# Kernel optimization log

Measured on AMD Instinct MI355X. Metric: run time of the kernel, lower is better.

Reference implementation:

```python
import jax, jax.numpy as jnp
import numpy as np

B, S, D, H = 4, 2048, 1024, 16
HD = D // H  # head_dim = 64


def setup_inputs() -> dict:
    key = jax.random.key(0)
    ks = jax.random.split(key, 9)
    sc = 0.02
    return {
        "x": jax.random.normal(ks[0], (B, S, D), dtype=jnp.float32),
        "mask": jnp.zeros((B, S), dtype=bool),  # True = masked
        "Wq": jax.random.normal(ks[1], (D, D), dtype=jnp.float32) * sc,
        "bq": jnp.zeros((D,), dtype=jnp.float32),
        "Wk": jax.random.normal(ks[2], (D, D), dtype=jnp.float32) * sc,
        "bk": jnp.zeros((D,), dtype=jnp.float32),
        "Wv": jax.random.normal(ks[3], (D, D), dtype=jnp.float32) * sc,
        "bv": jnp.zeros((D,), dtype=jnp.float32),
        "Wo": jax.random.normal(ks[4], (D, D), dtype=jnp.float32) * sc,
        "bo": jnp.zeros((D,), dtype=jnp.float32),
    }


def reference(x, mask, Wq, bq, Wk, bk, Wv, bv, Wo, bo):
    b, s, _ = x.shape
    scale = HD ** -0.5
    # projections, split heads: (b, h, s, hd)
    def heads(t):
        return t.reshape(b, s, H, HD).transpose(0, 2, 1, 3)
    q = heads(x @ Wq + bq)
    k = heads(x @ Wk + bk)
    v = heads(x @ Wv + bv)
    # scores: (b, h, s, s)
    attn = jnp.einsum('bhqd,bhkd->bhqk', q, k) * scale
    attn = jnp.where(mask[:, None, None, :], -jnp.inf, attn)
    attn = jax.nn.softmax(attn, axis=-1)
    # dropout p=0.0 -> identity (eval parity)
    out = jnp.einsum('bhqk,bhkd->bhqd', attn, v)
    out = out.transpose(0, 2, 1, 3).reshape(b, s, D)
    return out @ Wo + bo
```

## Files before the change

kernel.cpp:

```cpp
#include <hip/hip_runtime.h>
#include <cstdint>


typedef __bf16 bf16x8 __attribute__((ext_vector_type(8)));
typedef __bf16 bf16x4v __attribute__((ext_vector_type(4)));
typedef float f32x4 __attribute__((ext_vector_type(4)));
typedef unsigned u32x2 __attribute__((ext_vector_type(2)));
typedef unsigned u32x4 __attribute__((ext_vector_type(4)));

#define DEV __device__ __forceinline__

#if __has_builtin(__builtin_amdgcn_exp2f)
#define EXP2(x) __builtin_amdgcn_exp2f(x)
#else
#define EXP2(x) exp2f(x)
#endif

DEV __bf16 f2bf(float f) { return (__bf16)f; }

DEV void gload16(const void* g, void* l) {
  __builtin_amdgcn_global_load_lds(
      (const __attribute__((address_space(1))) unsigned int*)(uintptr_t)g,
      (__attribute__((address_space(3))) unsigned int*)(uintptr_t)l,
      16, 0, 0);
}

__global__ __launch_bounds__(256) void f2bf_vec4(const float4* __restrict__ in,
                                                 bf16x4v* __restrict__ out, int n4) {
  int i = blockIdx.x * blockDim.x + threadIdx.x;
  int stride = gridDim.x * blockDim.x;
  for (; i < n4; i += stride) {
    float4 v = in[i];
    bf16x4v o = { f2bf(v.x), f2bf(v.y), f2bf(v.z), f2bf(v.w) };
    out[i] = o;
  }
}

__global__ __launch_bounds__(256) void pack_mask(const unsigned char* __restrict__ mask,
                                                 unsigned* __restrict__ pm) {
  int t = threadIdx.x;
  int b = t >> 6, tile = (t >> 1) & 31, half = t & 1;
  unsigned bits = 0;
  for (int j = 0; j < 32; ++j)
    if (mask[b * 2048 + tile * 64 + half * 32 + j]) bits |= (1u << j);
  pm[b * 64 + tile * 2 + half] = bits;
}

__global__ __launch_bounds__(256) void pack_bias(const float* __restrict__ bq,
                                                 const float* __restrict__ bk,
                                                 const float* __restrict__ bv,
                                                 float* __restrict__ pb, float qs) {
  int i = blockIdx.x * 256 + threadIdx.x;
  float v = (i < 1024) ? bq[i] * qs : (i < 2048) ? bk[i - 1024] : bv[i - 2048];
  pb[i] = v;
}

__global__ __launch_bounds__(256) void transpose_w4(const float* __restrict__ w0,
                                                    const float* __restrict__ w1,
                                                    const float* __restrict__ w2,
                                                    const float* __restrict__ w3,
                                                    __bf16* __restrict__ dstb, float qs) {
  __shared__ float tile[32][33];
  const int which = blockIdx.z;
  const float* src = which == 0 ? w0 : which == 1 ? w1 : which == 2 ? w2 : w3;
  const float scale = (which == 0) ? qs : 1.0f;
  __bf16* dst = dstb + (size_t)which * 1024 * 1024;
  const int tx = threadIdx.x & 31;
  const int ty = threadIdx.x >> 5;
  const int x0 = blockIdx.x * 32;
  const int y0 = blockIdx.y * 32;
#pragma unroll
  for (int j = 0; j < 4; ++j)
    tile[ty + j * 8][tx] = src[(size_t)(y0 + ty + j * 8) * 1024 + x0 + tx];
  __syncthreads();
#pragma unroll
  for (int j = 0; j < 4; ++j)
    dst[(size_t)(x0 + ty + j * 8) * 1024 + y0 + tx] = f2bf(tile[tx][ty + j * 8] * scale);
}

__global__ __launch_bounds__(256, 2) void gemm128(const __bf16* __restrict__ A,
                                                  const __bf16* __restrict__ Bt,
                                                  const float* __restrict__ bias,
                                                  void* __restrict__ o0, void* __restrict__ o1,
                                                  void* __restrict__ o2, int mode) {
  constexpr int K = 1024;
  __shared__ alignas(16) __bf16 S[32768];
  const int t = threadIdx.x;
  const int lane = t & 63, w = t >> 6;
  const int g = lane >> 4, c = lane & 15;
  const int sw = c & 7;
  const int wm = w & 1, wn = w >> 1;
  const int bid = blockIdx.x;
  const int j = bid >> 3;
  const int m0 = (((bid & 7) << 3) + (j & 7)) << 7;
  const int n0 = (j >> 3) << 7;

  float bb4[4];
#pragma unroll
  for (int jj = 0; jj < 4; ++jj) bb4[jj] = bias[n0 + wn * 64 + jj * 16 + c];
  asm volatile("" :: "v"(bb4[0]), "v"(bb4[1]), "v"(bb4[2]), "v"(bb4[3]) : "memory");

  f32x4 acc[4][4];
#pragma unroll
  for (int i = 0; i < 4; ++i)
#pragma unroll
    for (int jj = 0; jj < 4; ++jj) acc[i][jj] = f32x4{0.f, 0.f, 0.f, 0.f};

  auto stage = [&](int bb, int k0) {
#pragma unroll
    for (int r2 = 0; r2 < 4; ++r2) {
      int slot = r2 * 256 + t;
      int row = slot >> 3, ch = slot & 7;
      int gch = ch ^ (row & 7);
      gload16(&A[(size_t)(m0 + row) * K + k0 + gch * 8], &S[bb * 8192 + slot * 8]);
      gload16(&Bt[(size_t)(n0 + row) * K + k0 + gch * 8], &S[16384 + bb * 8192 + slot * 8]);
    }
  };

  asm volatile("s_waitcnt vmcnt(0)" ::: "memory");
  stage(0, 0);

#pragma unroll 1
  for (int kt = 0; kt < 16; ++kt) {
    const int bb = kt & 1;
    if (kt < 15) {
      stage(bb ^ 1, (kt + 1) << 6);
      asm volatile("s_waitcnt vmcnt(8)" ::: "memory");
    } else {
      asm volatile("s_waitcnt vmcnt(0)" ::: "memory");
    }
    __builtin_amdgcn_s_barrier();

    const __bf16* As_ = S + bb * 8192;
    const __bf16* Bs_ = S + 16384 + bb * 8192;
    __builtin_amdgcn_s_setprio(1);
#pragma unroll
    for (int kk = 0; kk < 2; ++kk) {
      bf16x8 af[4], bfr[4];
#pragma unroll
      for (int i = 0; i < 4; ++i) {
        af[i]  = *(const bf16x8*)&As_[(wm * 64 + i * 16 + c) * 64 + (((kk * 4 + g) ^ sw) << 3)];
        bfr[i] = *(const bf16x8*)&Bs_[(wn * 64 + i * 16 + c) * 64 + (((kk * 4 + g) ^ sw) << 3)];
      }
#pragma unroll
      for (int i = 0; i < 4; ++i)
#pragma unroll
        for (int jj = 0; jj < 4; ++jj)
          acc[i][jj] = __builtin_amdgcn_mfma_f32_16x16x32_bf16(af[i], bfr[jj], acc[i][jj], 0, 0, 0);
    }
    __builtin_amdgcn_s_setprio(0);
    __builtin_amdgcn_s_barrier();
  }

  const int bidx = m0 >> 11;
  const int s0g = m0 & 2047;

  if (mode == 2) {
#pragma unroll
    for (int i = 0; i < 4; ++i) {
      const int rowb = m0 + wm * 64 + i * 16 + g * 4;
#pragma unroll
      for (int jj = 0; jj < 4; ++jj) {
        const int col = n0 + wn * 64 + jj * 16 + c;
#pragma unroll
        for (int r = 0; r < 4; ++r)
          ((float*)o0)[(size_t)(rowb + r) * 1024 + col] = acc[i][jj][r] + bb4[jj];
      }
    }
    return;
  }

  const int seg = n0 >> 10;
  const int hb = (n0 & 1023) >> 6;
  unsigned short* LB = (unsigned short*)S;

#pragma unroll
  for (int hh = 0; hh < 2; ++hh) {
    __syncthreads();
    if (wn == hh) {
#pragma unroll
      for (int i = 0; i < 4; ++i) {
        const int rl = wm * 64 + i * 16 + g * 4;
#pragma unroll
        for (int jj = 0; jj < 4; ++jj) {
          const int col = jj * 16 + c;
#pragma unroll
          for (int r = 0; r < 4; ++r) {
            const int row = rl + r;
            __bf16 v = f2bf(acc[i][jj][r] + bb4[jj]);
            if (seg < 2) {
              LB[row * 72 + col] = __builtin_bit_cast(unsigned short, v);
            } else {
              int spl = (row & 0x63) | ((row & 0x10) >> 2) | ((row & 0x0C) << 1);
              LB[col * 136 + spl] = __builtin_bit_cast(unsigned short, v);
            }
          }
        }
      }
    }
    __syncthreads();
    if (seg < 2) {
      __bf16* dst = (__bf16*)(seg == 0 ? o0 : o1);
      const size_t hbase = ((size_t)(bidx * 16 + hb + hh) * 2048 + s0g) * 64;
#pragma unroll
      for (int s4 = 0; s4 < 4; ++s4) {
        int row = s4 * 32 + (t >> 3);
        int hd0 = (t & 7) * 8;
        bf16x8 v = *(const bf16x8*)&LB[row * 72 + hd0];
        *(bf16x8*)&dst[hbase + (size_t)row * 64 + hd0] = v;
      }
    } else {
      __bf16* dst = (__bf16*)o2;
      const int hd = t >> 2, q4 = t & 3;
      const size_t vb = ((size_t)(bidx * 16 + hb + hh) * 64 + hd) * 2048 + s0g;
#pragma unroll
      for (int kk = 0; kk < 4; ++kk) {
        int spb = q4 * 32 + kk * 8;
        bf16x8 v = *(const bf16x8*)&LB[hd * 136 + spb];
        *(bf16x8*)&dst[vb + spb] = v;
      }
    }
  }
}

__global__ __launch_bounds__(256, 4) void attn_kernel(const __bf16* __restrict__ q,
                                                      const __bf16* __restrict__ k,
                                                      const __bf16* __restrict__ vt,
                                                      const unsigned* __restrict__ pm,
                                                      __bf16* __restrict__ outp) {
  const int bid = blockIdx.x;
  const int xcd = bid & 7, j = bid >> 3;
  const int bh = xcd * 8 + (j & 7), qb = j >> 3;
  const int b = bh >> 4, h = bh & 15;
  const int t = threadIdx.x, lane = t & 63, w = t >> 6;
  const int g = lane >> 4, c = lane & 15;
  const int sw = c & 7;

  __shared__ alignas(16) __bf16 S[12288];
  __bf16* Vs = S + 8192;

  const size_t kbase = (size_t)bh * (2048 * 64);
  const size_t vbase = (size_t)bh * (64 * 2048);
  const int q0 = qb * 128 + w * 32;

  unsigned mword = pm[b * 64 + lane];

  bf16x8 qf[2][2];
#pragma unroll
  for (int i = 0; i < 2; ++i)
#pragma unroll
    for (int m = 0; m < 2; ++m)
      qf[i][m] = *(const bf16x8*)&q[kbase + (size_t)(q0 + i * 16 + c) * 64 + m * 32 + g * 8];
  asm volatile("" :: "v"(qf[0][0]), "v"(qf[0][1]), "v"(qf[1][0]), "v"(qf[1][1]),
                     "v"(mword) : "memory");

  f32x4 acc[2][4];
  f32x4 lacc[2];
#pragma unroll
  for (int i = 0; i < 2; ++i) {
    lacc[i] = f32x4{0.f, 0.f, 0.f, 0.f};
#pragma unroll
    for (int n = 0; n < 4; ++n) acc[i][n] = f32x4{0.f, 0.f, 0.f, 0.f};
  }

  const bf16x8 ones = { (__bf16)1.f, (__bf16)1.f, (__bf16)1.f, (__bf16)1.f,
                        (__bf16)1.f, (__bf16)1.f, (__bf16)1.f, (__bf16)1.f };

  auto stageK = [&](int bb, int kv0) {
#pragma unroll
    for (int r2 = 0; r2 < 2; ++r2) {
      int slot = r2 * 256 + t;
      int row = slot >> 3, ch = slot & 7;
      int gch = ch ^ (row & 7);
      gload16(&k[kbase + (size_t)(kv0 + row) * 64 + gch * 8], &S[bb * 4096 + slot * 8]);
    }
  };
  auto stageV = [&](int kv0) {
#pragma unroll
    for (int r2 = 0; r2 < 2; ++r2) {
      int slot = r2 * 256 + t;
      int row = slot >> 3, ch = slot & 7;
      int gch = ch ^ (row & 7);
      gload16(&vt[vbase + (size_t)row * 2048 + kv0 + gch * 8], &Vs[slot * 8]);
    }
  };

  stageK(0, 0);
  stageV(0);

#pragma unroll 1
  for (int kv = 0; kv < 32; ++kv) {
    const int bb = kv & 1;
    const int kv0 = kv << 6;
    if (kv < 31) {
      stageK(bb ^ 1, kv0 + 64);
      asm volatile("s_waitcnt vmcnt(2)" ::: "memory");
    } else {
      asm volatile("s_waitcnt vmcnt(0)" ::: "memory");
    }
    __builtin_amdgcn_s_barrier();

    const __bf16* ksb = S + (bb << 12);
    unsigned mwlo = __builtin_amdgcn_readlane(mword, 2 * kv);
    unsigned mwhi = __builtin_amdgcn_readlane(mword, 2 * kv + 1);

    __builtin_amdgcn_s_setprio(1);
    f32x4 sc[2][4];
#pragma unroll
    for (int n = 0; n < 4; ++n) {
      bf16x8 kf0 = *(const bf16x8*)&ksb[(n * 16 + c) * 64 + (((0 + g) ^ sw) << 3)];
      bf16x8 kf1 = *(const bf16x8*)&ksb[(n * 16 + c) * 64 + (((4 + g) ^ sw) << 3)];
#pragma unroll
      for (int i = 0; i < 2; ++i) {
        f32x4 z = f32x4{0.f, 0.f, 0.f, 0.f};
        z = __builtin_amdgcn_mfma_f32_16x16x32_bf16(kf0, qf[i][0], z, 0, 0, 0);
        z = __builtin_amdgcn_mfma_f32_16x16x32_bf16(kf1, qf[i][1], z, 0, 0, 0);
        sc[i][n] = z;
      }
    }
    __builtin_amdgcn_sched_barrier(0);

    u32x4 pf0[2];
    if (mwlo) {
#pragma unroll
      for (int n = 0; n < 2; ++n)
#pragma unroll
        for (int r = 0; r < 4; ++r)
          if ((mwlo >> (n * 16 + g * 4 + r)) & 1u) { sc[0][n][r] = -1e30f; sc[1][n][r] = -1e30f; }
    }
#pragma unroll
    for (int i = 0; i < 2; ++i) {
      float p0 = EXP2(sc[i][0][0]), p1 = EXP2(sc[i][0][1]);
      float p2 = EXP2(sc[i][0][2]), p3 = EXP2(sc[i][0][3]);
      float p4 = EXP2(sc[i][1][0]), p5 = EXP2(sc[i][1][1]);
      float p6 = EXP2(sc[i][1][2]), p7 = EXP2(sc[i][1][3]);
      unsigned w0, w1, w2, w3;
      asm("v_cvt_pk_bf16_f32 %0, %1, %2" : "=v"(w0) : "v"(p0), "v"(p1));
      asm("v_cvt_pk_bf16_f32 %0, %1, %2" : "=v"(w1) : "v"(p2), "v"(p3));
      asm("v_cvt_pk_bf16_f32 %0, %1, %2" : "=v"(w2) : "v"(p4), "v"(p5));
      asm("v_cvt_pk_bf16_f32 %0, %1, %2" : "=v"(w3) : "v"(p6), "v"(p7));
      pf0[i] = u32x4{w0, w1, w2, w3};
    }

#pragma unroll
    for (int n = 0; n < 4; ++n) {
      bf16x8 vf0 = *(const bf16x8*)&Vs[(n * 16 + c) * 64 + (((0 + g) ^ sw) << 3)];
#pragma unroll
      for (int i = 0; i < 2; ++i)
        acc[i][n] = __builtin_amdgcn_mfma_f32_16x16x32_bf16(vf0, __builtin_bit_cast(bf16x8, pf0[i]), acc[i][n], 0, 0, 0);
    }
#pragma unroll
    for (int i = 0; i < 2; ++i)
      lacc[i] = __builtin_amdgcn_mfma_f32_16x16x32_bf16(ones, __builtin_bit_cast(bf16x8, pf0[i]), lacc[i], 0, 0, 0);
    __builtin_amdgcn_sched_barrier(0);

    u32x4 pf1[2];
    if (mwhi) {
#pragma unroll
      for (int n = 2; n < 4; ++n)
#pragma unroll
        for (int r = 0; r < 4; ++r)
          if ((mwhi >> ((n - 2) * 16 + g * 4 + r)) & 1u) { sc[0][n][r] = -1e30f; sc[1][n][r] = -1e30f; }
    }
#pragma unroll
    for (int i = 0; i < 2; ++i) {
      float p0 = EXP2(sc[i][2][0]), p1 = EXP2(sc[i][2][1]);
      float p2 = EXP2(sc[i][2][2]), p3 = EXP2(sc[i][2][3]);
      float p4 = EXP2(sc[i][3][0]), p5 = EXP2(sc[i][3][1]);
      float p6 = EXP2(sc[i][3][2]), p7 = EXP2(sc[i][3][3]);
      unsigned w0, w1, w2, w3;
      asm("v_cvt_pk_bf16_f32 %0, %1, %2" : "=v"(w0) : "v"(p0), "v"(p1));
      asm("v_cvt_pk_bf16_f32 %0, %1, %2" : "=v"(w1) : "v"(p2), "v"(p3));
      asm("v_cvt_pk_bf16_f32 %0, %1, %2" : "=v"(w2) : "v"(p4), "v"(p5));
      asm("v_cvt_pk_bf16_f32 %0, %1, %2" : "=v"(w3) : "v"(p6), "v"(p7));
      pf1[i] = u32x4{w0, w1, w2, w3};
    }

#pragma unroll
    for (int n = 0; n < 4; ++n) {
      bf16x8 vf1 = *(const bf16x8*)&Vs[(n * 16 + c) * 64 + (((4 + g) ^ sw) << 3)];
#pragma unroll
      for (int i = 0; i < 2; ++i)
        acc[i][n] = __builtin_amdgcn_mfma_f32_16x16x32_bf16(vf1, __builtin_bit_cast(bf16x8, pf1[i]), acc[i][n], 0, 0, 0);
    }
#pragma unroll
    for (int i = 0; i < 2; ++i)
      lacc[i] = __builtin_amdgcn_mfma_f32_16x16x32_bf16(ones, __builtin_bit_cast(bf16x8, pf1[i]), lacc[i], 0, 0, 0);
    __builtin_amdgcn_s_setprio(0);

    __builtin_amdgcn_s_barrier();
    if (kv < 31) stageV(kv0 + 64);
  }

  float linv[2];
#pragma unroll
  for (int i = 0; i < 2; ++i) linv[i] = 1.0f / fmaxf(lacc[i][0], 1e-30f);

  __bf16* ot = S + w * 2176;
#pragma unroll
  for (int i = 0; i < 2; ++i)
#pragma unroll
    for (int n = 0; n < 4; ++n) {
      float a0 = acc[i][n][0] * linv[i], a1 = acc[i][n][1] * linv[i];
      float a2 = acc[i][n][2] * linv[i], a3 = acc[i][n][3] * linv[i];
      unsigned w0, w1;
      asm("v_cvt_pk_bf16_f32 %0, %1, %2" : "=v"(w0) : "v"(a0), "v"(a1));
      asm("v_cvt_pk_bf16_f32 %0, %1, %2" : "=v"(w1) : "v"(a2), "v"(a3));
      *(u32x2*)&ot[(i * 16 + c) * 68 + n * 16 + g * 4] = u32x2{w0, w1};
    }
  asm volatile("s_waitcnt lgkmcnt(0)" ::: "memory");
  __builtin_amdgcn_sched_barrier(0);
#pragma unroll
  for (int ps = 0; ps < 4; ++ps) {
    int rr = ps * 8 + (lane >> 3);
    bf16x8 ov = *(const bf16x8*)&ot[rr * 68 + (lane & 7) * 8];
    *(bf16x8*)&outp[((size_t)b * 2048 + q0 + rr) * 1024 + h * 64 + (lane & 7) * 8] = ov;
  }
}

extern "C" void kernel_launch(void* const* d_in, const int* in_sizes, int n_in,
                              void* d_out, int out_size, void* d_ws, size_t ws_size,
                              hipStream_t stream) {
  (void)in_sizes; (void)n_in; (void)out_size; (void)ws_size;
  const float* x  = (const float*)d_in[0];
  const unsigned char* mask = (const unsigned char*)d_in[1];
  const float* Wq = (const float*)d_in[2];
  const float* bq = (const float*)d_in[3];
  const float* Wk = (const float*)d_in[4];
  const float* bk = (const float*)d_in[5];
  const float* Wv = (const float*)d_in[6];
  const float* bv = (const float*)d_in[7];
  const float* Wo = (const float*)d_in[8];
  const float* bo = (const float*)d_in[9];
  float* out = (float*)d_out;

  char* ws = (char*)d_ws;
  const size_t SZ = (size_t)8192 * 1024 * 2;
  const size_t WSZ = (size_t)1024 * 1024 * 2;
  __bf16* xb  = (__bf16*)(ws);
  __bf16* qb  = (__bf16*)(ws + SZ);
  __bf16* kb  = (__bf16*)(ws + 2 * SZ);
  __bf16* vtb = (__bf16*)(ws + 3 * SZ);
  __bf16* wtq = (__bf16*)(ws + 4 * SZ);
  __bf16* wto = (__bf16*)(ws + 4 * SZ + 3 * WSZ);
  unsigned* pmask = (unsigned*)(ws + 4 * SZ + 4 * WSZ);
  float* pb = (float*)(ws + 4 * SZ + 4 * WSZ + 4096);

  const float QSCALE = 0.125f * 1.44269504f;

  f2bf_vec4<<<2048, 256, 0, stream>>>((const float4*)x, (bf16x4v*)xb, 8192 * 1024 / 4);
  pack_mask<<<1, 256, 0, stream>>>(mask, pmask);
  pack_bias<<<12, 256, 0, stream>>>(bq, bk, bv, pb, QSCALE);
  transpose_w4<<<dim3(32, 32, 4), 256, 0, stream>>>(Wq, Wk, Wv, Wo, wtq, QSCALE);
  gemm128<<<dim3(1536), 256, 0, stream>>>(xb, wtq, pb, qb, kb, vtb, 3);
  attn_kernel<<<dim3(1024), 256, 0, stream>>>(qb, kb, vtb, pmask, xb);
  gemm128<<<dim3(512), 256, 0, stream>>>(xb, wto, bo, out, nullptr, nullptr, 2);
}
```

Before: 180.3 us.

## Switch GEMMs to 256x128 tiles with 512 threads and triple-buffered LDS

Replaces the 128x128 GEMM with a 256x128 tile computed by 8 waves. It uses a three-stage LDS ring (dynamic shared memory, 144KB) and splits each K-step into four MFMA quarters, with interleaved global loads and barriers between them. The XCD-aware block mapping is rewritten around a per-GEMM column-block count, and the transposed-V epilogue is adapted to the taller tile. The aim is better operand reuse and deeper prefetch to hide load latency, at the cost of one block per CU from the LDS footprint and more barriers per K-step.

```diff
diff --git a/kernel.cpp b/kernel.cpp
--- a/kernel.cpp
+++ b/kernel.cpp
@@ -24,6 +24,8 @@
       (__attribute__((address_space(3))) unsigned int*)(uintptr_t)l,
       16, 0, 0);
 }
+
+#define MFMA16(a, b, c) __builtin_amdgcn_mfma_f32_16x16x32_bf16((a), (b), (c), 0, 0, 0)
 
 __global__ __launch_bounds__(256) void f2bf_vec4(const float4* __restrict__ in,
                                                  bf16x4v* __restrict__ out, int n4) {
@@ -78,22 +80,26 @@
     dst[(size_t)(x0 + ty + j * 8) * 1024 + y0 + tx] = f2bf(tile[tx][ty + j * 8] * scale);
 }
 
-__global__ __launch_bounds__(256, 2) void gemm128(const __bf16* __restrict__ A,
+__global__ __launch_bounds__(512, 2) void gemm256(const __bf16* __restrict__ A,
                                                   const __bf16* __restrict__ Bt,
                                                   const float* __restrict__ bias,
                                                   void* __restrict__ o0, void* __restrict__ o1,
-                                                  void* __restrict__ o2, int mode) {
+                                                  void* __restrict__ o2,
+                                                  int nbn, int mode) {
+  extern __shared__ __align__(16) char smem_raw[];
+  __bf16* S = (__bf16*)smem_raw;
   constexpr int K = 1024;
-  __shared__ alignas(16) __bf16 S[32768];
   const int t = threadIdx.x;
   const int lane = t & 63, w = t >> 6;
   const int g = lane >> 4, c = lane & 15;
   const int sw = c & 7;
-  const int wm = w & 1, wn = w >> 1;
+  const int wm = w & 3, wn = w >> 2;
   const int bid = blockIdx.x;
-  const int j = bid >> 3;
-  const int m0 = (((bid & 7) << 3) + (j & 7)) << 7;
-  const int n0 = (j >> 3) << 7;
+  const int xcd = bid & 7, j0 = bid >> 3;
+  const int mb = xcd * 4 + j0 / nbn;
+  const int nb = j0 % nbn;
+  const int m0 = mb << 8;
+  const int n0 = nb << 7;
 
   float bb4[4];
 #pragma unroll
@@ -106,54 +112,117 @@
 #pragma unroll
     for (int jj = 0; jj < 4; ++jj) acc[i][jj] = f32x4{0.f, 0.f, 0.f, 0.f};
 
-  auto stage = [&](int bb, int k0) {
-#pragma unroll
-    for (int r2 = 0; r2 < 4; ++r2) {
-      int slot = r2 * 256 + t;
-      int row = slot >> 3, ch = slot & 7;
-      int gch = ch ^ (row & 7);
-      gload16(&A[(size_t)(m0 + row) * K + k0 + gch * 8], &S[bb * 8192 + slot * 8]);
-      gload16(&Bt[(size_t)(n0 + row) * K + k0 + gch * 8], &S[16384 + bb * 8192 + slot * 8]);
+  auto stA = [&](int bufe, int k0, int h) {
+#pragma unroll
+    for (int r2 = 0; r2 < 2; ++r2) {
+      int slot = r2 * 512 + t;
+      int row = slot >> 3;
+      int gch = (slot & 7) ^ (row & 7);
+      gload16(&A[(size_t)(m0 + h * 128 + row) * K + k0 + gch * 8],
+              &S[bufe + h * 8192 + slot * 8]);
     }
   };
+  auto stB = [&](int bufe, int k0, int h) {
+    int row = t >> 3;
+    int gch = (t & 7) ^ (row & 7);
+    gload16(&Bt[(size_t)(n0 + h * 64 + row) * K + k0 + gch * 8],
+            &S[bufe + 16384 + h * 4096 + t * 8]);
+  };
 
   asm volatile("s_waitcnt vmcnt(0)" ::: "memory");
-  stage(0, 0);
+  stA(0, 0, 0); stA(0, 0, 1); stB(0, 0, 0); stB(0, 0, 1);
+  stA(24576, 64, 0); stA(24576, 64, 1); stB(24576, 64, 0); stB(24576, 64, 1);
+
+  const int arow = wm * 64 + c;
+  const int brow = wn * 64 + c;
 
 #pragma unroll 1
   for (int kt = 0; kt < 16; ++kt) {
-    const int bb = kt & 1;
-    if (kt < 15) {
-      stage(bb ^ 1, (kt + 1) << 6);
+    const int cb = (kt % 3) * 24576;
+    const int pb2 = ((kt + 2) % 3) * 24576;
+    const int k0p = (kt + 2) << 6;
+    const __bf16* Ab = S + cb;
+    const __bf16* Bb = S + cb + 16384;
+    bf16x8 af[2][2], b01[2][2], b23[2][2];
+
+    if (kt < 14) {
+      stA(pb2, k0p, 0);
       asm volatile("s_waitcnt vmcnt(8)" ::: "memory");
+    } else if (kt == 14) {
+      asm volatile("s_waitcnt vmcnt(6)" ::: "memory");
     } else {
       asm volatile("s_waitcnt vmcnt(0)" ::: "memory");
     }
     __builtin_amdgcn_s_barrier();
-
-    const __bf16* As_ = S + bb * 8192;
-    const __bf16* Bs_ = S + 16384 + bb * 8192;
+#pragma unroll
+    for (int i = 0; i < 2; ++i)
+#pragma unroll
+      for (int kk = 0; kk < 2; ++kk)
+        af[i][kk] = *(const bf16x8*)&Ab[(arow + i * 16) * 64 + (((kk * 4 + g) ^ sw) << 3)];
+#pragma unroll
+    for (int jn = 0; jn < 2; ++jn)
+#pragma unroll
+      for (int kk = 0; kk < 2; ++kk)
+        b01[jn][kk] = *(const bf16x8*)&Bb[(brow + jn * 16) * 64 + (((kk * 4 + g) ^ sw) << 3)];
     __builtin_amdgcn_s_setprio(1);
 #pragma unroll
-    for (int kk = 0; kk < 2; ++kk) {
-      bf16x8 af[4], bfr[4];
-#pragma unroll
-      for (int i = 0; i < 4; ++i) {
-        af[i]  = *(const bf16x8*)&As_[(wm * 64 + i * 16 + c) * 64 + (((kk * 4 + g) ^ sw) << 3)];
-        bfr[i] = *(const bf16x8*)&Bs_[(wn * 64 + i * 16 + c) * 64 + (((kk * 4 + g) ^ sw) << 3)];
-      }
-#pragma unroll
-      for (int i = 0; i < 4; ++i)
-#pragma unroll
-        for (int jj = 0; jj < 4; ++jj)
-          acc[i][jj] = __builtin_amdgcn_mfma_f32_16x16x32_bf16(af[i], bfr[jj], acc[i][jj], 0, 0, 0);
-    }
+    for (int kk = 0; kk < 2; ++kk)
+#pragma unroll
+      for (int i = 0; i < 2; ++i)
+#pragma unroll
+        for (int jn = 0; jn < 2; ++jn)
+          acc[i][jn] = MFMA16(af[i][kk], b01[jn][kk], acc[i][jn]);
     __builtin_amdgcn_s_setprio(0);
+
+    if (kt < 14) stA(pb2, k0p, 1);
+    asm volatile("" ::: "memory");
     __builtin_amdgcn_s_barrier();
-  }
-
-  const int bidx = m0 >> 11;
-  const int s0g = m0 & 2047;
+#pragma unroll
+    for (int jn = 0; jn < 2; ++jn)
+#pragma unroll
+      for (int kk = 0; kk < 2; ++kk)
+        b23[jn][kk] = *(const bf16x8*)&Bb[(brow + (jn + 2) * 16) * 64 + (((kk * 4 + g) ^ sw) << 3)];
+    __builtin_amdgcn_s_setprio(1);
+#pragma unroll
+    for (int kk = 0; kk < 2; ++kk)
+#pragma unroll
+      for (int i = 0; i < 2; ++i)
+#pragma unroll
+        for (int jn = 0; jn < 2; ++jn)
+          acc[i][jn + 2] = MFMA16(af[i][kk], b23[jn][kk], acc[i][jn + 2]);
+    __builtin_amdgcn_s_setprio(0);
+
+    if (kt < 14) stB(pb2, k0p, 0);
+    asm volatile("" ::: "memory");
+    __builtin_amdgcn_s_barrier();
+#pragma unroll
+    for (int i = 0; i < 2; ++i)
+#pragma unroll
+      for (int kk = 0; kk < 2; ++kk)
+        af[i][kk] = *(const bf16x8*)&Ab[(arow + (i + 2) * 16) * 64 + (((kk * 4 + g) ^ sw) << 3)];
+    __builtin_amdgcn_s_setprio(1);
+#pragma unroll
+    for (int kk = 0; kk < 2; ++kk)
+#pragma unroll
+      for (int i = 0; i < 2; ++i)
+#pragma unroll
+        for (int jn = 0; jn < 2; ++jn)
+          acc[i + 2][jn] = MFMA16(af[i][kk], b01[jn][kk], acc[i + 2][jn]);
+    __builtin_amdgcn_s_setprio(0);
+
+    if (kt < 14) stB(pb2, k0p, 1);
+    asm volatile("" ::: "memory");
+    __builtin_amdgcn_s_barrier();
+    __builtin_amdgcn_s_setprio(1);
+#pragma unroll
+    for (int kk = 0; kk < 2; ++kk)
+#pragma unroll
+      for (int i = 0; i < 2; ++i)
+#pragma unroll
+        for (int jn = 0; jn < 2; ++jn)
+          acc[i + 2][jn + 2] = MFMA16(af[i][kk], b23[jn][kk], acc[i + 2][jn + 2]);
+    __builtin_amdgcn_s_setprio(0);
+  }
 
   if (mode == 2) {
 #pragma unroll
@@ -172,6 +241,8 @@
 
   const int seg = n0 >> 10;
   const int hb = (n0 & 1023) >> 6;
+  const int bidx = m0 >> 11;
+  const int s0g = m0 & 2047;
   unsigned short* LB = (unsigned short*)S;
 
 #pragma unroll
@@ -191,8 +262,8 @@
             if (seg < 2) {
               LB[row * 72 + col] = __builtin_bit_cast(unsigned short, v);
             } else {
-              int spl = (row & 0x63) | ((row & 0x10) >> 2) | ((row & 0x0C) << 1);
-              LB[col * 136 + spl] = __builtin_bit_cast(unsigned short, v);
+              int spl = (row & ~0x1C) | ((row & 0x0C) << 1) | ((row & 0x10) >> 2);
+              LB[col * 264 + spl] = __builtin_bit_cast(unsigned short, v);
             }
           }
         }
@@ -204,20 +275,19 @@
       const size_t hbase = ((size_t)(bidx * 16 + hb + hh) * 2048 + s0g) * 64;
 #pragma unroll
       for (int s4 = 0; s4 < 4; ++s4) {
-        int row = s4 * 32 + (t >> 3);
+        int row = s4 * 64 + (t >> 3);
         int hd0 = (t & 7) * 8;
         bf16x8 v = *(const bf16x8*)&LB[row * 72 + hd0];
         *(bf16x8*)&dst[hbase + (size_t)row * 64 + hd0] = v;
       }
     } else {
       __bf16* dst = (__bf16*)o2;
-      const int hd = t >> 2, q4 = t & 3;
-      const size_t vb = ((size_t)(bidx * 16 + hb + hh) * 64 + hd) * 2048 + s0g;
-#pragma unroll
-      for (int kk = 0; kk < 4; ++kk) {
-        int spb = q4 * 32 + kk * 8;
-        bf16x8 v = *(const bf16x8*)&LB[hd * 136 + spb];
-        *(bf16x8*)&dst[vb + spb] = v;
+#pragma unroll
+      for (int p = 0; p < 4; ++p) {
+        int hd = p * 16 + (t >> 5);
+        int sl = (t & 31) * 8;
+        bf16x8 v = *(const bf16x8*)&LB[hd * 264 + sl];
+        *(bf16x8*)&dst[((size_t)(bidx * 16 + hb + hh) * 64 + hd) * 2048 + s0g + sl] = v;
       }
     }
   }
@@ -313,8 +383,8 @@
 #pragma unroll
       for (int i = 0; i < 2; ++i) {
         f32x4 z = f32x4{0.f, 0.f, 0.f, 0.f};
-        z = __builtin_amdgcn_mfma_f32_16x16x32_bf16(kf0, qf[i][0], z, 0, 0, 0);
-        z = __builtin_amdgcn_mfma_f32_16x16x32_bf16(kf1, qf[i][1], z, 0, 0, 0);
+        z = MFMA16(kf0, qf[i][0], z);
+        z = MFMA16(kf1, qf[i][1], z);
         sc[i][n] = z;
       }
     }
@@ -347,11 +417,11 @@
       bf16x8 vf0 = *(const bf16x8*)&Vs[(n * 16 + c) * 64 + (((0 + g) ^ sw) << 3)];
 #pragma unroll
       for (int i = 0; i < 2; ++i)
-        acc[i][n] = __builtin_amdgcn_mfma_f32_16x16x32_bf16(vf0, __builtin_bit_cast(bf16x8, pf0[i]), acc[i][n], 0, 0, 0);
+        acc[i][n] = MFMA16(vf0, __builtin_bit_cast(bf16x8, pf0[i]), acc[i][n]);
     }
 #pragma unroll
     for (int i = 0; i < 2; ++i)
-      lacc[i] = __builtin_amdgcn_mfma_f32_16x16x32_bf16(ones, __builtin_bit_cast(bf16x8, pf0[i]), lacc[i], 0, 0, 0);
+      lacc[i] = MFMA16(ones, __builtin_bit_cast(bf16x8, pf0[i]), lacc[i]);
     __builtin_amdgcn_sched_barrier(0);
 
     u32x4 pf1[2];
@@ -381,11 +451,11 @@
       bf16x8 vf1 = *(const bf16x8*)&Vs[(n * 16 + c) * 64 + (((4 + g) ^ sw) << 3)];
 #pragma unroll
       for (int i = 0; i < 2; ++i)
-        acc[i][n] = __builtin_amdgcn_mfma_f32_16x16x32_bf16(vf1, __builtin_bit_cast(bf16x8, pf1[i]), acc[i][n], 0, 0, 0);
+        acc[i][n] = MFMA16(vf1, __builtin_bit_cast(bf16x8, pf1[i]), acc[i][n]);
     }
 #pragma unroll
     for (int i = 0; i < 2; ++i)
-      lacc[i] = __builtin_amdgcn_mfma_f32_16x16x32_bf16(ones, __builtin_bit_cast(bf16x8, pf1[i]), lacc[i], 0, 0, 0);
+      lacc[i] = MFMA16(ones, __builtin_bit_cast(bf16x8, pf1[i]), lacc[i]);
     __builtin_amdgcn_s_setprio(0);
 
     __builtin_amdgcn_s_barrier();
@@ -447,12 +517,13 @@
   float* pb = (float*)(ws + 4 * SZ + 4 * WSZ + 4096);
 
   const float QSCALE = 0.125f * 1.44269504f;
+  const int LDSB = 147456;
 
   f2bf_vec4<<<2048, 256, 0, stream>>>((const float4*)x, (bf16x4v*)xb, 8192 * 1024 / 4);
   pack_mask<<<1, 256, 0, stream>>>(mask, pmask);
   pack_bias<<<12, 256, 0, stream>>>(bq, bk, bv, pb, QSCALE);
   transpose_w4<<<dim3(32, 32, 4), 256, 0, stream>>>(Wq, Wk, Wv, Wo, wtq, QSCALE);
-  gemm128<<<dim3(1536), 256, 0, stream>>>(xb, wtq, pb, qb, kb, vtb, 3);
+  gemm256<<<dim3(768), 512, LDSB, stream>>>(xb, wtq, pb, qb, kb, vtb, 24, 3);
   attn_kernel<<<dim3(1024), 256, 0, stream>>>(qb, kb, vtb, pmask, xb);
-  gemm128<<<dim3(512), 256, 0, stream>>>(xb, wto, bo, out, nullptr, nullptr, 2);
-}
+  gemm256<<<dim3(256), 512, LDSB, stream>>>(xb, wto, bo, out, nullptr, nullptr, 8, 2);
+}
```

Result: slower. 184.1 us (+2.1%).

## Single-buffer GEMM shared memory to raise occupancy to four blocks per CU

Applied to the files above, without the earlier changes.

Replaces the double-buffered LDS staging in the projection GEMM with a single 32 KB buffer and plain __syncthreads, and raises launch bounds from 2 to 4 blocks per CU. The aim is to hide global-load latency through more resident waves instead of software prefetch, and it drops the setprio hints. The trade-off is that loads and MFMA work within a block no longer overlap, and four blocks per CU caps each thread at a smaller register budget, which may force spills of the 64-float accumulator. The other edits only add an MFMA macro and reorder the bit-swizzle expression.

```diff
diff --git a/kernel.cpp b/kernel.cpp
--- a/kernel.cpp
+++ b/kernel.cpp
@@ -24,6 +24,8 @@
       (__attribute__((address_space(3))) unsigned int*)(uintptr_t)l,
       16, 0, 0);
 }
+
+#define MFMA16(a, b, c) __builtin_amdgcn_mfma_f32_16x16x32_bf16((a), (b), (c), 0, 0, 0)
 
 __global__ __launch_bounds__(256) void f2bf_vec4(const float4* __restrict__ in,
                                                  bf16x4v* __restrict__ out, int n4) {
@@ -78,13 +80,15 @@
     dst[(size_t)(x0 + ty + j * 8) * 1024 + y0 + tx] = f2bf(tile[tx][ty + j * 8] * scale);
 }
 
-__global__ __launch_bounds__(256, 2) void gemm128(const __bf16* __restrict__ A,
+__global__ __launch_bounds__(256, 4) void gemm128(const __bf16* __restrict__ A,
                                                   const __bf16* __restrict__ Bt,
                                                   const float* __restrict__ bias,
                                                   void* __restrict__ o0, void* __restrict__ o1,
                                                   void* __restrict__ o2, int mode) {
   constexpr int K = 1024;
-  __shared__ alignas(16) __bf16 S[32768];
+  __shared__ alignas(16) __bf16 S[16384];
+  __bf16* As_ = S;
+  __bf16* Bs_ = S + 8192;
   const int t = threadIdx.x;
   const int lane = t & 63, w = t >> 6;
   const int g = lane >> 4, c = lane & 15;
@@ -98,42 +102,25 @@
   float bb4[4];
 #pragma unroll
   for (int jj = 0; jj < 4; ++jj) bb4[jj] = bias[n0 + wn * 64 + jj * 16 + c];
-  asm volatile("" :: "v"(bb4[0]), "v"(bb4[1]), "v"(bb4[2]), "v"(bb4[3]) : "memory");
 
   f32x4 acc[4][4];
 #pragma unroll
   for (int i = 0; i < 4; ++i)
 #pragma unroll
     for (int jj = 0; jj < 4; ++jj) acc[i][jj] = f32x4{0.f, 0.f, 0.f, 0.f};
-
-  auto stage = [&](int bb, int k0) {
-#pragma unroll
-    for (int r2 = 0; r2 < 4; ++r2) {
-      int slot = r2 * 256 + t;
-      int row = slot >> 3, ch = slot & 7;
-      int gch = ch ^ (row & 7);
-      gload16(&A[(size_t)(m0 + row) * K + k0 + gch * 8], &S[bb * 8192 + slot * 8]);
-      gload16(&Bt[(size_t)(n0 + row) * K + k0 + gch * 8], &S[16384 + bb * 8192 + slot * 8]);
-    }
-  };
-
-  asm volatile("s_waitcnt vmcnt(0)" ::: "memory");
-  stage(0, 0);
 
 #pragma unroll 1
   for (int kt = 0; kt < 16; ++kt) {
-    const int bb = kt & 1;
-    if (kt < 15) {
-      stage(bb ^ 1, (kt + 1) << 6);
-      asm volatile("s_waitcnt vmcnt(8)" ::: "memory");
-    } else {
-      asm volatile("s_waitcnt vmcnt(0)" ::: "memory");
-    }
-    __builtin_amdgcn_s_barrier();
-
-    const __bf16* As_ = S + bb * 8192;
-    const __bf16* Bs_ = S + 16384 + bb * 8192;
-    __builtin_amdgcn_s_setprio(1);
+    const int k0 = kt << 6;
+#pragma unroll
+    for (int i = 0; i < 4; ++i) {
+      int slot = i * 256 + t;
+      int row = slot >> 3;
+      int gch = (slot & 7) ^ (row & 7);
+      gload16(&A[(size_t)(m0 + row) * K + k0 + gch * 8], &As_[slot * 8]);
+      gload16(&Bt[(size_t)(n0 + row) * K + k0 + gch * 8], &Bs_[slot * 8]);
+    }
+    __syncthreads();
 #pragma unroll
     for (int kk = 0; kk < 2; ++kk) {
       bf16x8 af[4], bfr[4];
@@ -146,10 +133,9 @@
       for (int i = 0; i < 4; ++i)
 #pragma unroll
         for (int jj = 0; jj < 4; ++jj)
-          acc[i][jj] = __builtin_amdgcn_mfma_f32_16x16x32_bf16(af[i], bfr[jj], acc[i][jj], 0, 0, 0);
-    }
-    __builtin_amdgcn_s_setprio(0);
-    __builtin_amdgcn_s_barrier();
+          acc[i][jj] = MFMA16(af[i], bfr[jj], acc[i][jj]);
+    }
+    __syncthreads();
   }
 
   const int bidx = m0 >> 11;
@@ -191,7 +177,7 @@
             if (seg < 2) {
               LB[row * 72 + col] = __builtin_bit_cast(unsigned short, v);
             } else {
-              int spl = (row & 0x63) | ((row & 0x10) >> 2) | ((row & 0x0C) << 1);
+              int spl = (row & ~0x1C) | ((row & 0x0C) << 1) | ((row & 0x10) >> 2);
               LB[col * 136 + spl] = __builtin_bit_cast(unsigned short, v);
             }
           }
@@ -313,8 +299,8 @@
 #pragma unroll
       for (int i = 0; i < 2; ++i) {
         f32x4 z = f32x4{0.f, 0.f, 0.f, 0.f};
-        z = __builtin_amdgcn_mfma_f32_16x16x32_bf16(kf0, qf[i][0], z, 0, 0, 0);
-        z = __builtin_amdgcn_mfma_f32_16x16x32_bf16(kf1, qf[i][1], z, 0, 0, 0);
+        z = MFMA16(kf0, qf[i][0], z);
+        z = MFMA16(kf1, qf[i][1], z);
         sc[i][n] = z;
       }
     }
@@ -347,11 +333,11 @@
       bf16x8 vf0 = *(const bf16x8*)&Vs[(n * 16 + c) * 64 + (((0 + g) ^ sw) << 3)];
 #pragma unroll
       for (int i = 0; i < 2; ++i)
-        acc[i][n] = __builtin_amdgcn_mfma_f32_16x16x32_bf16(vf0, __builtin_bit_cast(bf16x8, pf0[i]), acc[i][n], 0, 0, 0);
+        acc[i][n] = MFMA16(vf0, __builtin_bit_cast(bf16x8, pf0[i]), acc[i][n]);
     }
 #pragma unroll
     for (int i = 0; i < 2; ++i)
-      lacc[i] = __builtin_amdgcn_mfma_f32_16x16x32_bf16(ones, __builtin_bit_cast(bf16x8, pf0[i]), lacc[i], 0, 0, 0);
+      lacc[i] = MFMA16(ones, __builtin_bit_cast(bf16x8, pf0[i]), lacc[i]);
     __builtin_amdgcn_sched_barrier(0);
 
     u32x4 pf1[2];
@@ -381,11 +367,11 @@
       bf16x8 vf1 = *(const bf16x8*)&Vs[(n * 16 + c) * 64 + (((4 + g) ^ sw) << 3)];
 #pragma unroll
       for (int i = 0; i < 2; ++i)
-        acc[i][n] = __builtin_amdgcn_mfma_f32_16x16x32_bf16(vf1, __builtin_bit_cast(bf16x8, pf1[i]), acc[i][n], 0, 0, 0);
+        acc[i][n] = MFMA16(vf1, __builtin_bit_cast(bf16x8, pf1[i]), acc[i][n]);
     }
 #pragma unroll
     for (int i = 0; i < 2; ++i)
-      lacc[i] = __builtin_amdgcn_mfma_f32_16x16x32_bf16(ones, __builtin_bit_cast(bf16x8, pf1[i]), lacc[i], 0, 0, 0);
+      lacc[i] = MFMA16(ones, __builtin_bit_cast(bf16x8, pf1[i]), lacc[i]);
     __builtin_amdgcn_s_setprio(0);
 
     __builtin_amdgcn_s_barrier();
```

Result: faster. 173.8 us (-3.6%).
